# Kernel tuning notes

Hardware: AMD Instinct MI355X
Metric: run time of the kernel (lower is better)

The kernel has to match this reference:

```python
import jax, jax.numpy as jnp
import numpy as np

BANDLIMIT = 0.5
STEP_SCALE = 1.0  # refiner default step_scale_value
LN_EPS = 1e-5


def _layernorm(x, g, b):
    mu = jnp.mean(x, axis=-1, keepdims=True)
    xc = x - mu
    inv = jax.lax.rsqrt(jnp.mean(xc * xc, axis=-1, keepdims=True) + LN_EPS)
    return xc * inv * g + b


def setup_inputs() -> dict:
    key = jax.random.key(0)
    ks = jax.random.split(key, 12)
    B, C, H, W = 16, 384, 64, 64
    P = 192  # conj-sym half of state_dim=384
    x = jax.random.normal(ks[0], (B, C, H, W), dtype=jnp.float32)
    ln1_g = 1.0 + 0.1 * jax.random.normal(ks[1], (C,), dtype=jnp.float32)
    ln1_b = 0.1 * jax.random.normal(ks[2], (C,), dtype=jnp.float32)
    # stable diagonal A: negative real part, HiPPO-like imaginary ladder
    lam_re = -(0.3 + jax.random.uniform(ks[3], (P,), dtype=jnp.float32))
    lam_im = jnp.pi * jnp.arange(P, dtype=jnp.float32)
    Lambda = jnp.stack([lam_re, lam_im], axis=-1)          # [P,2] (re,im)
    Bmat = jax.random.normal(ks[4], (P, C, 2), dtype=jnp.float32) / np.sqrt(C)
    Cmat = jax.random.normal(ks[5], (C, P, 2), dtype=jnp.float32) / np.sqrt(P)
    D = jax.random.normal(ks[6], (C,), dtype=jnp.float32)
    log_step = jax.random.uniform(ks[7], (P,), dtype=jnp.float32,
                                  minval=float(np.log(1e-3)), maxval=float(np.log(0.1)))
    ln2_g = 1.0 + 0.1 * jax.random.normal(ks[8], (C,), dtype=jnp.float32)
    ln2_b = 0.1 * jax.random.normal(ks[9], (C,), dtype=jnp.float32)
    W_enc = jax.random.normal(ks[10], (2 * C, C), dtype=jnp.float32) / np.sqrt(C)
    W_dec = jax.random.normal(ks[11], (C, C), dtype=jnp.float32) / np.sqrt(C)
    return {"x": x, "ln1_g": ln1_g, "ln1_b": ln1_b, "Lambda": Lambda,
            "Bmat": Bmat, "Cmat": Cmat, "D": D, "log_step": log_step,
            "ln2_g": ln2_g, "ln2_b": ln2_b, "W_enc": W_enc, "W_dec": W_dec}


def reference(x, ln1_g, ln1_b, Lambda, Bmat, Cmat, D, log_step, ln2_g, ln2_b, W_enc, W_dec):
    Bsz, C, H, W = x.shape
    u = x.reshape(Bsz, C, H * W).transpose(0, 2, 1)        # [B, L, C]

    # --- S5Block: attn branch ---
    fx = _layernorm(u, ln1_g, ln1_b)
    res = fx

    lam = Lambda[..., 0] + 1j * Lambda[..., 1]             # [P] complex
    Bc = Bmat[..., 0] + 1j * Bmat[..., 1]                  # [P, C]
    Cc = Cmat[..., 0] + 1j * Cmat[..., 1]                  # [C, P]
    step = STEP_SCALE * jnp.exp(log_step)                  # [P]
    # bandlimit mask on C (as in S5 with bandlimit=0.5)
    freqs = (step / STEP_SCALE) * jnp.abs(Lambda[..., 1]) / (2.0 * jnp.pi)
    mask = (freqs < BANDLIMIT * 0.5).astype(Cc.dtype)
    Cc = Cc * mask
    # ZOH discretization
    lam_bar = jnp.exp(lam * step)                          # [P]
    B_bar = ((lam_bar - 1.0) / lam)[:, None] * Bc          # [P, C]
    Bu = jnp.einsum('ph,blh->blp', B_bar, fx.astype(B_bar.dtype))  # [B,L,P] complex
    lam_el = jnp.broadcast_to(lam_bar, Bu.shape)

    def binop(a, b):
        # linear recurrence composition: x <- a2*(a1*x + b1) + b2
        return a[0] * b[0], b[0] * a[1] + b[1]

    _, xs = jax.lax.associative_scan(binop, (lam_el, Bu), axis=1)  # [B,L,P]
    y = 2.0 * jnp.real(jnp.einsum('hp,blp->blh', Cc, xs)) + D * fx
    y = jax.nn.gelu(y, approximate=False) + res

    # --- S5Block: GEGLU FFN branch ---
    fy = _layernorm(y, ln2_g, ln2_b)
    z = fy @ W_enc.T                                       # [B,L,2C]
    z1, z2 = jnp.split(z, 2, axis=-1)
    z = z1 * jax.nn.gelu(z2, approximate=False)
    y = z @ W_dec.T + fy

    return y.transpose(0, 2, 1).reshape(Bsz, C, H, W)
```

## Files before the change

kernel.cpp:

```cpp
#include <hip/hip_runtime.h>
#include <hip/hip_bf16.h>
#include <math.h>

typedef __attribute__((ext_vector_type(4))) float f32x4;
typedef __attribute__((ext_vector_type(8))) short s16x8;
typedef unsigned short u16;
typedef unsigned int u32;

#define CDIM 384
#define PDIM 192
#define LDIM 4096
#define BSZ  16
#define MDIM 65536
#define KD   384
#define BM 128
#define BN 128
#define BK 32
#define NT (KD / BK)

__device__ __forceinline__ u16 f2bf(float f) {
    u32 x = __float_as_uint(f);
    x += 0x7fffu + ((x >> 16) & 1u);
    return (u16)(x >> 16);
}
__device__ __forceinline__ float bf2f(u16 v) {
    return __uint_as_float(((u32)v) << 16);
}
__device__ __forceinline__ float gelu_exact(float x) {
    return 0.5f * x * (1.0f + erff(x * 0.7071067811865476f));
}
__device__ __forceinline__ float gelu_fast(float x) {
    float w = -1.5957691216f * x * (1.0f + 0.044715f * x * x);
    return x / (1.0f + __expf(w));
}
__device__ __forceinline__ void gld_lds16(const u16* g, u16* l) {
    __builtin_amdgcn_global_load_lds(
        (const __attribute__((address_space(1))) void*)g,
        (__attribute__((address_space(3))) void*)l, 16, 0, 0);
}

__device__ __forceinline__ void swz_decode(int NY, int& mt, int& nt) {
    int bid = blockIdx.x + gridDim.x * blockIdx.y;
    int nwg = gridDim.x * gridDim.y;
    int cpx = nwg >> 3;
    int work = (bid & 7) * cpx + (bid >> 3);
    mt = work / NY;
    nt = work - mt * NY;
}

__global__ __launch_bounds__(256) void k_setup(
    const float* __restrict__ Lambda, const float* __restrict__ Bmat,
    const float* __restrict__ Cmat, const float* __restrict__ log_step,
    const float* __restrict__ W_enc, const float* __restrict__ W_dec,
    u16* __restrict__ Wb, u16* __restrict__ Wc, u16* __restrict__ We,
    u16* __restrict__ Wd, float* __restrict__ lam_bar)
{
    int idx = blockIdx.x * 256 + threadIdx.x;
    if (idx < 73728) {
        int p = idx / CDIM, c = idx % CDIM;
        float st  = expf(log_step[p]);
        float lre = Lambda[2*p], lim = Lambda[2*p+1];
        float el  = expf(lre * st);
        float lbr = el * cosf(lim * st);
        float lbi = el * sinf(lim * st);
        float dd  = lre*lre + lim*lim;
        float a = lbr - 1.0f, b = lbi;
        float cr = (a * lre + b * lim) / dd;
        float ci = (b * lre - a * lim) / dd;
        float Br = Bmat[2*(p*CDIM + c)], Bi = Bmat[2*(p*CDIM + c) + 1];
        Wb[p*KD + c]          = f2bf(cr*Br - ci*Bi);
        Wb[(PDIM + p)*KD + c] = f2bf(cr*Bi + ci*Br);
    } else if (idx < 147456) {
        int e = idx - 73728;
        int h = e / PDIM, p = e % PDIM;
        float st  = expf(log_step[p]);
        float lim = Lambda[2*p+1];
        float freq = st * fabsf(lim) / 6.283185307179586f;
        float sc = (freq < 0.25f) ? 2.0f : 0.0f;
        Wc[h*KD + p]        = f2bf( sc * Cmat[2*(h*PDIM + p)]);
        Wc[h*KD + PDIM + p] = f2bf(-sc * Cmat[2*(h*PDIM + p) + 1]);
    } else if (idx < 442368) {
        int e = idx - 147456;
        We[e] = f2bf(W_enc[e]);
    } else if (idx < 589824) {
        int e = idx - 442368;
        Wd[e] = f2bf(W_dec[e]);
    } else if (idx < 590016) {
        int p = idx - 589824;
        float st  = expf(log_step[p]);
        float lre = Lambda[2*p], lim = Lambda[2*p+1];
        float el  = expf(lre * st);
        lam_bar[2*p]   = el * cosf(lim * st);
        lam_bar[2*p+1] = el * sinf(lim * st);
    }
}

__global__ __launch_bounds__(256) void k_ln1(
    const float* __restrict__ x, const float* __restrict__ g,
    const float* __restrict__ bb, u16* __restrict__ fx)
{
    __shared__ float tile[CDIM * 36];
    __shared__ float mu_sh[32], inv_sh[32];
    int b  = blockIdx.x >> 7;
    int l0 = (blockIdx.x & 127) * 32;
    int tid = threadIdx.x;
    const float* src = x + ((size_t)b * CDIM) * LDIM + l0;
    #pragma unroll
    for (int it = 0; it < 12; it++) {
        int s = it * 256 + tid;
        int ch = s >> 3, c4 = (s & 7) * 4;
        float4 v = *(const float4*)(src + (size_t)ch * LDIM + c4);
        *(float4*)(tile + ch * 36 + c4) = v;
    }
    __syncthreads();
    int j = tid >> 3, k = tid & 7;
    float sum = 0.f, sq = 0.f;
    for (int c = k; c < CDIM; c += 8) {
        float v = tile[c * 36 + j];
        sum += v; sq += v * v;
    }
    sum += __shfl_xor(sum, 1); sq += __shfl_xor(sq, 1);
    sum += __shfl_xor(sum, 2); sq += __shfl_xor(sq, 2);
    sum += __shfl_xor(sum, 4); sq += __shfl_xor(sq, 4);
    float mu  = sum * (1.0f / CDIM);
    float var = sq * (1.0f / CDIM) - mu * mu;
    float inv = rsqrtf(var + 1e-5f);
    if (k == 0) { mu_sh[j] = mu; inv_sh[j] = inv; }
    __syncthreads();
    u16* dst = fx + ((size_t)(b * LDIM + l0)) * CDIM;
    #pragma unroll
    for (int it = 0; it < 12; it++) {
        int s  = it * 256 + tid;
        int cq = s % 96, jj = s / 96;
        int c  = cq * 4;
        float m2 = mu_sh[jj], iv = inv_sh[jj];
        float4 gv = *(const float4*)(g + c);
        float4 bv = *(const float4*)(bb + c);
        ushort4 o;
        o.x = f2bf((tile[(c+0)*36 + jj] - m2) * iv * gv.x + bv.x);
        o.y = f2bf((tile[(c+1)*36 + jj] - m2) * iv * gv.y + bv.y);
        o.z = f2bf((tile[(c+2)*36 + jj] - m2) * iv * gv.z + bv.z);
        o.w = f2bf((tile[(c+3)*36 + jj] - m2) * iv * gv.w + bv.w);
        *(ushort4*)(dst + (size_t)jj * CDIM + c) = o;
    }
}

template<bool SWAP>
__device__ __forceinline__ void gemm_core(
    const u16* __restrict__ A, int lda, const u16* __restrict__ Bw,
    int m0, int n0, u16* a_sh, u16* b_sh, f32x4 acc[4][4])
{
    const int tid  = threadIdx.x;
    const int w    = tid >> 6, lane = tid & 63;
    const int t16  = lane & 15, quad = lane >> 4;
    const int wm   = w >> 1,   wn   = w & 1;
    const int lr  = lane >> 2;
    const int cbg = (lane & 3) ^ ((lane >> 3) & 3);
    const u16* gA0 = A  + (size_t)(m0 + w*32 + lr) * lda + cbg*8;
    const u16* gA1 = gA0 + (size_t)16 * lda;
    const u16* gB0 = Bw + (size_t)(n0 + w*32 + lr) * KD + cbg*8;
    const u16* gB1 = gB0 + (size_t)16 * KD;
    u16* lA0 = a_sh + (w*32) * BK;
    u16* lA1 = lA0 + 16*BK;
    u16* lB0 = b_sh + (w*32) * BK;
    u16* lB1 = lB0 + 16*BK;
    const int pos = (quad ^ ((t16 >> 1) & 3)) * 8;
    const u16* ard = a_sh + (wm*64 + t16) * BK + pos;
    const u16* brd = b_sh + (wn*64 + t16) * BK + pos;
    #pragma unroll
    for (int i = 0; i < 4; i++)
        #pragma unroll
        for (int j = 0; j < 4; j++) acc[i][j] = (f32x4){0.f,0.f,0.f,0.f};
    gld_lds16(gA0, lA0);
    gld_lds16(gA1, lA1);
    gld_lds16(gB0, lB0);
    gld_lds16(gB1, lB1);
    int cur = 0;
    #pragma unroll 2
    for (int t = 0; t < NT; ++t) {
        __syncthreads();
        if (t + 1 < NT) {
            int kb = (t + 1) * BK;
            int nxt = cur ^ 1;
            gld_lds16(gA0 + kb, lA0 + nxt * (BM*BK));
            gld_lds16(gA1 + kb, lA1 + nxt * (BM*BK));
            gld_lds16(gB0 + kb, lB0 + nxt * (BN*BK));
            gld_lds16(gB1 + kb, lB1 + nxt * (BN*BK));
        }
        const u16* ac = ard + cur * (BM*BK);
        const u16* bc = brd + cur * (BN*BK);
        s16x8 af[4], bfr[4];
        #pragma unroll
        for (int i = 0; i < 4; i++) af[i]  = *(const s16x8*)(ac + i*16*BK);
        #pragma unroll
        for (int j = 0; j < 4; j++) bfr[j] = *(const s16x8*)(bc + j*16*BK);
        #pragma unroll
        for (int i = 0; i < 4; i++)
            #pragma unroll
            for (int j = 0; j < 4; j++) {
                if (SWAP)
                    acc[i][j] = __builtin_amdgcn_mfma_f32_16x16x32_bf16(bfr[j], af[i], acc[i][j], 0,0,0);
                else
                    acc[i][j] = __builtin_amdgcn_mfma_f32_16x16x32_bf16(af[i], bfr[j], acc[i][j], 0,0,0);
            }
        cur ^= 1;
    }
}

__global__ __launch_bounds__(256) void k_gemm_bu(
    const u16* __restrict__ fx, const u16* __restrict__ Wb, u16* __restrict__ Bu)
{
    __shared__ __align__(16) u16 a_sh[2*BM*BK], b_sh[2*BN*BK];
    int mt, nt;
    swz_decode(gridDim.y, mt, nt);
    int m0 = mt * BM, n0 = nt * BN;
    f32x4 acc[4][4];
    gemm_core<false>(fx, CDIM, Wb, m0, n0, a_sh, b_sh, acc);
    int lane = threadIdx.x & 63, w = threadIdx.x >> 6;
    int t16 = lane & 15, quad = lane >> 4, wm = w >> 1, wn = w & 1;
    #pragma unroll
    for (int i = 0; i < 4; i++)
        #pragma unroll
        for (int j = 0; j < 4; j++)
            #pragma unroll
            for (int rr = 0; rr < 4; rr++) {
                int m = m0 + wm*64 + i*16 + quad*4 + rr;
                int n = n0 + wn*64 + j*16 + t16;
                Bu[(size_t)m * CDIM + n] = f2bf(acc[i][j][rr]);
            }
}

__global__ __launch_bounds__(256) void k_gemm_y(
    const u16* __restrict__ xs, const u16* __restrict__ Wc,
    const u16* __restrict__ fx, const float* __restrict__ Dv, u16* __restrict__ y)
{
    __shared__ __align__(16) u16 a_sh[2*BM*BK], b_sh[2*BN*BK];
    int mt, nt;
    swz_decode(gridDim.y, mt, nt);
    int m0 = mt * BM, n0 = nt * BN;
    f32x4 acc[4][4];
    gemm_core<false>(xs, CDIM, Wc, m0, n0, a_sh, b_sh, acc);
    int lane = threadIdx.x & 63, w = threadIdx.x >> 6;
    int t16 = lane & 15, quad = lane >> 4, wm = w >> 1, wn = w & 1;
    float dv[4];
    #pragma unroll
    for (int j = 0; j < 4; j++) dv[j] = Dv[n0 + wn*64 + j*16 + t16];
    #pragma unroll
    for (int i = 0; i < 4; i++)
        #pragma unroll
        for (int j = 0; j < 4; j++)
            #pragma unroll
            for (int rr = 0; rr < 4; rr++) {
                int m = m0 + wm*64 + i*16 + quad*4 + rr;
                int n = n0 + wn*64 + j*16 + t16;
                float fxv = bf2f(fx[(size_t)m * CDIM + n]);
                float v = acc[i][j][rr] + dv[j] * fxv;
                y[(size_t)m * CDIM + n] = f2bf(gelu_fast(v) + fxv);
            }
}

__global__ __launch_bounds__(256) void k_gemm_zg(
    const u16* __restrict__ fy, const u16* __restrict__ We, u16* __restrict__ zg)
{
    __shared__ __align__(16) u16 sh[4*BM*BK];
    u16* a_sh = sh;
    u16* b_sh = sh + 2*BM*BK;
    const int tid = threadIdx.x;
    const int w = tid >> 6, lane = tid & 63;
    const int t16 = lane & 15, quad = lane >> 4;
    const int wm = w >> 1, wn = w & 1;
    int mt, nt;
    swz_decode(gridDim.y, mt, nt);
    const int m0 = mt * BM;
    const int c0 = nt * 64;
    const int lr  = lane >> 2;
    const int cbg = (lane & 3) ^ ((lane >> 3) & 3);
    const u16* gA0 = fy + (size_t)(m0 + w*32 + lr) * CDIM + cbg*8;
    const u16* gA1 = gA0 + (size_t)16 * CDIM;
    int brow = c0 + w*32 + ((w >= 2) ? 320 : 0);
    const u16* gB0 = We + (size_t)(brow + lr) * KD + cbg*8;
    const u16* gB1 = gB0 + (size_t)16 * KD;
    u16* lA0 = a_sh + (w*32) * BK;
    u16* lA1 = lA0 + 16*BK;
    u16* lB0 = b_sh + (w*32) * BK;
    u16* lB1 = lB0 + 16*BK;
    const int pos = (quad ^ ((t16 >> 1) & 3)) * 8;
    const u16* ard = a_sh + (wm*64 + t16) * BK + pos;
    const u16* brd = b_sh + (wn*64 + t16) * BK + pos;
    f32x4 acc[4][4];
    #pragma unroll
    for (int i = 0; i < 4; i++)
        #pragma unroll
        for (int j = 0; j < 4; j++) acc[i][j] = (f32x4){0.f,0.f,0.f,0.f};
    gld_lds16(gA0, lA0);
    gld_lds16(gA1, lA1);
    gld_lds16(gB0, lB0);
    gld_lds16(gB1, lB1);
    int cur = 0;
    #pragma unroll 2
    for (int t = 0; t < NT; ++t) {
        __syncthreads();
        if (t + 1 < NT) {
            int kb = (t + 1) * BK;
            int nxt = cur ^ 1;
            gld_lds16(gA0 + kb, lA0 + nxt * (BM*BK));
            gld_lds16(gA1 + kb, lA1 + nxt * (BM*BK));
            gld_lds16(gB0 + kb, lB0 + nxt * (BN*BK));
            gld_lds16(gB1 + kb, lB1 + nxt * (BN*BK));
        }
        const u16* ac = ard + cur * (BM*BK);
        const u16* bc = brd + cur * (BN*BK);
        s16x8 af[4], bfr[4];
        #pragma unroll
        for (int i = 0; i < 4; i++) af[i]  = *(const s16x8*)(ac + i*16*BK);
        #pragma unroll
        for (int j = 0; j < 4; j++) bfr[j] = *(const s16x8*)(bc + j*16*BK);
        #pragma unroll
        for (int i = 0; i < 4; i++)
            #pragma unroll
            for (int j = 0; j < 4; j++)
                acc[i][j] = __builtin_amdgcn_mfma_f32_16x16x32_bf16(af[i], bfr[j], acc[i][j], 0,0,0);
        cur ^= 1;
    }
    __syncthreads();
    if (wn == 1) {
        #pragma unroll
        for (int i = 0; i < 4; i++)
            #pragma unroll
            for (int j = 0; j < 4; j++)
                #pragma unroll
                for (int rr = 0; rr < 4; rr++) {
                    int m = wm*64 + i*16 + quad*4 + rr;
                    int c = j*16 + t16;
                    sh[m*66 + c] = f2bf(gelu_fast(acc[i][j][rr]));
                }
    }
    __syncthreads();
    if (wn == 0) {
        #pragma unroll
        for (int i = 0; i < 4; i++)
            #pragma unroll
            for (int j = 0; j < 4; j++)
                #pragma unroll
                for (int rr = 0; rr < 4; rr++) {
                    int m = wm*64 + i*16 + quad*4 + rr;
                    int c = j*16 + t16;
                    float gv = bf2f(sh[m*66 + c]);
                    zg[(size_t)(m0 + m) * CDIM + c0 + c] = f2bf(acc[i][j][rr] * gv);
                }
    }
}

__global__ __launch_bounds__(256) void k_gemm_out(
    const u16* __restrict__ zg, const u16* __restrict__ Wd,
    const u16* __restrict__ fy, float* __restrict__ out)
{
    __shared__ __align__(16) u16 a_sh[2*BM*BK], b_sh[2*BN*BK];
    int mt, nt;
    swz_decode(gridDim.y, mt, nt);
    int m0 = mt * BM, n0 = nt * BN;
    f32x4 acc[4][4];
    gemm_core<true>(zg, CDIM, Wd, m0, n0, a_sh, b_sh, acc);
    int lane = threadIdx.x & 63, w = threadIdx.x >> 6;
    int t16 = lane & 15, quad = lane >> 4, wm = w >> 1, wn = w & 1;
    int b = m0 >> 12;
    #pragma unroll
    for (int i = 0; i < 4; i++)
        #pragma unroll
        for (int j = 0; j < 4; j++)
            #pragma unroll
            for (int rr = 0; rr < 4; rr++) {
                int nn = n0 + wn*64 + j*16 + quad*4 + rr;
                int mm = m0 + wm*64 + i*16 + t16;
                float fyv = bf2f(fy[(size_t)mm * CDIM + nn]);
                int l = mm & 4095;
                out[((size_t)(b * CDIM + nn)) * LDIM + l] = acc[i][j][rr] + fyv;
            }
}

__global__ __launch_bounds__(192) void k_scan_a(
    const u16* __restrict__ Bu, const float* __restrict__ lam_bar,
    float* __restrict__ summ)
{
    int b = blockIdx.x >> 6, ch = blockIdx.x & 63;
    int p = threadIdx.x;
    float lr = lam_bar[2*p], li = lam_bar[2*p+1];
    float xr = 0.f, xi = 0.f;
    const u16* base = Bu + (size_t)(b * LDIM + ch * 64) * CDIM;
    #pragma unroll 8
    for (int i = 0; i < 64; i++) {
        float br = bf2f(base[(size_t)i * CDIM + p]);
        float bi = bf2f(base[(size_t)i * CDIM + PDIM + p]);
        float nr = lr * xr - li * xi + br;
        float ni = lr * xi + li * xr + bi;
        xr = nr; xi = ni;
    }
    size_t o = (size_t)(b * 64 + ch) * CDIM + p;
    summ[o] = xr;
    summ[o + PDIM] = xi;
}

__global__ __launch_bounds__(256) void k_scan_b(
    const float* __restrict__ lam_bar, float* __restrict__ summ)
{
    int id = blockIdx.x * 256 + threadIdx.x;
    if (id >= BSZ * PDIM) return;
    int b = id / PDIM, p = id % PDIM;
    float ar = lam_bar[2*p], ai = lam_bar[2*p+1];
    #pragma unroll
    for (int s = 0; s < 6; s++) {
        float nr = ar * ar - ai * ai, ni = 2.f * ar * ai;
        ar = nr; ai = ni;
    }
    float cr = 0.f, ci = 0.f;
    #pragma unroll 4
    for (int ch = 0; ch < 64; ch++) {
        size_t o = (size_t)(b * 64 + ch) * CDIM + p;
        float sr = summ[o], si = summ[o + PDIM];
        summ[o] = cr; summ[o + PDIM] = ci;
        float nr = ar * cr - ai * ci + sr;
        float ni = ar * ci + ai * cr + si;
        cr = nr; ci = ni;
    }
}

__global__ __launch_bounds__(192) void k_scan_c(
    u16* __restrict__ Bu, const float* __restrict__ lam_bar,
    const float* __restrict__ summ)
{
    int b = blockIdx.x >> 6, ch = blockIdx.x & 63;
    int p = threadIdx.x;
    float lr = lam_bar[2*p], li = lam_bar[2*p+1];
    size_t oc = (size_t)(b * 64 + ch) * CDIM + p;
    float xr = summ[oc], xi = summ[oc + PDIM];
    u16* base = Bu + (size_t)(b * LDIM + ch * 64) * CDIM;
    #pragma unroll 8
    for (int i = 0; i < 64; i++) {
        float br = bf2f(base[(size_t)i * CDIM + p]);
        float bi = bf2f(base[(size_t)i * CDIM + PDIM + p]);
        float nr = lr * xr - li * xi + br;
        float ni = lr * xi + li * xr + bi;
        xr = nr; xi = ni;
        base[(size_t)i * CDIM + p] = f2bf(xr);
        base[(size_t)i * CDIM + PDIM + p] = f2bf(xi);
    }
}

__global__ __launch_bounds__(256) void k_ln2(
    const u16* __restrict__ y, const float* __restrict__ g,
    const float* __restrict__ bb, u16* __restrict__ fy)
{
    int w = threadIdx.x >> 6, lane = threadIdx.x & 63;
    size_t m = (size_t)blockIdx.x * 4 + w;
    const u16* row = y + m * CDIM;
    float v[6];
    float sum = 0.f, sq = 0.f;
    #pragma unroll
    for (int i = 0; i < 6; i++) {
        v[i] = bf2f(row[lane + 64 * i]);
        sum += v[i]; sq += v[i] * v[i];
    }
    #pragma unroll
    for (int o = 1; o < 64; o <<= 1) {
        sum += __shfl_xor(sum, o); sq += __shfl_xor(sq, o);
    }
    float mu  = sum * (1.0f / CDIM);
    float var = sq * (1.0f / CDIM) - mu * mu;
    float inv = rsqrtf(var + 1e-5f);
    u16* dst = fy + m * CDIM;
    #pragma unroll
    for (int i = 0; i < 6; i++) {
        int c = lane + 64 * i;
        dst[c] = f2bf((v[i] - mu) * inv * g[c] + bb[c]);
    }
}

extern "C" void kernel_launch(void* const* d_in, const int* in_sizes, int n_in,
                              void* d_out, int out_size, void* d_ws, size_t ws_size,
                              hipStream_t stream)
{
    const float* x        = (const float*)d_in[0];
    const float* ln1_g    = (const float*)d_in[1];
    const float* ln1_b    = (const float*)d_in[2];
    const float* Lambda   = (const float*)d_in[3];
    const float* Bmat     = (const float*)d_in[4];
    const float* Cmat     = (const float*)d_in[5];
    const float* Dvec     = (const float*)d_in[6];
    const float* log_step = (const float*)d_in[7];
    const float* ln2_g    = (const float*)d_in[8];
    const float* ln2_b    = (const float*)d_in[9];
    const float* W_enc    = (const float*)d_in[10];
    const float* W_dec    = (const float*)d_in[11];

    char* ws = (char*)d_ws;
    const size_t HBF = (size_t)MDIM * CDIM * 2;
    u16* fx = (u16*)(ws);
    u16* fy = (u16*)(ws + HBF);
    u16* bu = (u16*)(ws + 2 * HBF);
    u16* zg = (u16*)(ws + 2 * HBF);
    char* wbase = ws + 3 * HBF;
    u16* Wb = (u16*)(wbase);
    u16* Wc = (u16*)(wbase + 294912);
    u16* We = (u16*)(wbase + 589824);
    u16* Wd = (u16*)(wbase + 1179648);
    float* lam_bar = (float*)(wbase + 1474560);
    float* summ    = (float*)(wbase + 1476096);
    u16* yb  = (u16*)d_out;
    float* out = (float*)d_out;

    k_setup<<<2305, 256, 0, stream>>>(Lambda, Bmat, Cmat, log_step, W_enc, W_dec,
                                      Wb, Wc, We, Wd, lam_bar);
    k_ln1<<<2048, 256, 0, stream>>>(x, ln1_g, ln1_b, fx);
    k_gemm_bu<<<dim3(512, 3), 256, 0, stream>>>(fx, Wb, bu);
    k_scan_a<<<1024, 192, 0, stream>>>(bu, lam_bar, summ);
    k_scan_b<<<12, 256, 0, stream>>>(lam_bar, summ);
    k_scan_c<<<1024, 192, 0, stream>>>(bu, lam_bar, summ);
    k_gemm_y<<<dim3(512, 3), 256, 0, stream>>>(bu, Wc, fx, Dvec, yb);
    k_ln2<<<16384, 256, 0, stream>>>(yb, ln2_g, ln2_b, fy);
    k_gemm_zg<<<dim3(512, 6), 256, 0, stream>>>(fy, We, zg);
    k_gemm_out<<<dim3(512, 3), 256, 0, stream>>>(zg, Wd, fy, out);
}
```

Measured before the change: 447.0 us.

## Triple-buffer LDS tiles with two-stage-ahead prefetch in GEMM kernels

Replaces the double-buffered K loop in the shared GEMM core and the fused encoder GEMM with a three-buffer ring, prefetching tile t+2 while computing tile t. Explicit vmcnt waits plus a raw s_barrier replace __syncthreads, so the loads for the next tile can stay in flight across the barrier and global latency is hidden better. The cost is 50% more LDS per block, which may lower occupancy, and the handwritten waitcnt counts depend on the exact number of outstanding loads per thread. A strange null-pointer ternary was also added to the B-fragment loads in the encoder kernel.

Result: faster. 428.0 us (-4.3%).

```diff
diff --git a/kernel.cpp b/kernel.cpp
--- a/kernel.cpp
+++ b/kernel.cpp
@@ -17,6 +17,7 @@
 #define BN 128
 #define BK 32
 #define NT (KD / BK)
+#define BUFE (BM * BK)
 
 __device__ __forceinline__ u16 f2bf(float f) {
     u32 x = __float_as_uint(f);
@@ -175,20 +176,27 @@
     gld_lds16(gA1, lA1);
     gld_lds16(gB0, lB0);
     gld_lds16(gB1, lB1);
-    int cur = 0;
-    #pragma unroll 2
+    gld_lds16(gA0 + BK, lA0 + BUFE);
+    gld_lds16(gA1 + BK, lA1 + BUFE);
+    gld_lds16(gB0 + BK, lB0 + BUFE);
+    gld_lds16(gB1 + BK, lB1 + BUFE);
+    #pragma unroll
     for (int t = 0; t < NT; ++t) {
-        __syncthreads();
-        if (t + 1 < NT) {
-            int kb = (t + 1) * BK;
-            int nxt = cur ^ 1;
-            gld_lds16(gA0 + kb, lA0 + nxt * (BM*BK));
-            gld_lds16(gA1 + kb, lA1 + nxt * (BM*BK));
-            gld_lds16(gB0 + kb, lB0 + nxt * (BN*BK));
-            gld_lds16(gB1 + kb, lB1 + nxt * (BN*BK));
+        if (t < NT - 1) asm volatile("s_waitcnt vmcnt(4)" ::: "memory");
+        else            asm volatile("s_waitcnt vmcnt(0)" ::: "memory");
+        __builtin_amdgcn_s_barrier();
+        __builtin_amdgcn_sched_barrier(0);
+        if (t + 2 < NT) {
+            const int kb = (t + 2) * BK;
+            const int bo = ((t + 2) % 3) * BUFE;
+            gld_lds16(gA0 + kb, lA0 + bo);
+            gld_lds16(gA1 + kb, lA1 + bo);
+            gld_lds16(gB0 + kb, lB0 + bo);
+            gld_lds16(gB1 + kb, lB1 + bo);
         }
-        const u16* ac = ard + cur * (BM*BK);
-        const u16* bc = brd + cur * (BN*BK);
+        __builtin_amdgcn_sched_barrier(0);
+        const u16* ac = ard + (t % 3) * BUFE;
+        const u16* bc = brd + (t % 3) * BUFE;
         s16x8 af[4], bfr[4];
         #pragma unroll
         for (int i = 0; i < 4; i++) af[i]  = *(const s16x8*)(ac + i*16*BK);
@@ -203,14 +211,13 @@
                 else
                     acc[i][j] = __builtin_amdgcn_mfma_f32_16x16x32_bf16(af[i], bfr[j], acc[i][j], 0,0,0);
             }
-        cur ^= 1;
     }
 }
 
 __global__ __launch_bounds__(256) void k_gemm_bu(
     const u16* __restrict__ fx, const u16* __restrict__ Wb, u16* __restrict__ Bu)
 {
-    __shared__ __align__(16) u16 a_sh[2*BM*BK], b_sh[2*BN*BK];
+    __shared__ __align__(16) u16 a_sh[3*BUFE], b_sh[3*BUFE];
     int mt, nt;
     swz_decode(gridDim.y, mt, nt);
     int m0 = mt * BM, n0 = nt * BN;
@@ -234,7 +241,7 @@
     const u16* __restrict__ xs, const u16* __restrict__ Wc,
     const u16* __restrict__ fx, const float* __restrict__ Dv, u16* __restrict__ y)
 {
-    __shared__ __align__(16) u16 a_sh[2*BM*BK], b_sh[2*BN*BK];
+    __shared__ __align__(16) u16 a_sh[3*BUFE], b_sh[3*BUFE];
     int mt, nt;
     swz_decode(gridDim.y, mt, nt);
     int m0 = mt * BM, n0 = nt * BN;
@@ -262,9 +269,9 @@
 __global__ __launch_bounds__(256) void k_gemm_zg(
     const u16* __restrict__ fy, const u16* __restrict__ We, u16* __restrict__ zg)
 {
-    __shared__ __align__(16) u16 sh[4*BM*BK];
+    __shared__ __align__(16) u16 sh[6*BUFE];
     u16* a_sh = sh;
-    u16* b_sh = sh + 2*BM*BK;
+    u16* b_sh = sh + 3*BUFE;
     const int tid = threadIdx.x;
     const int w = tid >> 6, lane = tid & 63;
     const int t16 = lane & 15, quad = lane >> 4;
@@ -296,31 +303,37 @@
     gld_lds16(gA1, lA1);
     gld_lds16(gB0, lB0);
     gld_lds16(gB1, lB1);
-    int cur = 0;
-    #pragma unroll 2
+    gld_lds16(gA0 + BK, lA0 + BUFE);
+    gld_lds16(gA1 + BK, lA1 + BUFE);
+    gld_lds16(gB0 + BK, lB0 + BUFE);
+    gld_lds16(gB1 + BK, lB1 + BUFE);
+    #pragma unroll
     for (int t = 0; t < NT; ++t) {
-        __syncthreads();
-        if (t + 1 < NT) {
-            int kb = (t + 1) * BK;
-            int nxt = cur ^ 1;
-            gld_lds16(gA0 + kb, lA0 + nxt * (BM*BK));
-            gld_lds16(gA1 + kb, lA1 + nxt * (BM*BK));
-            gld_lds16(gB0 + kb, lB0 + nxt * (BN*BK));
-            gld_lds16(gB1 + kb, lB1 + nxt * (BN*BK));
+        if (t < NT - 1) asm volatile("s_waitcnt vmcnt(4)" ::: "memory");
+        else            asm volatile("s_waitcnt vmcnt(0)" ::: "memory");
+        __builtin_amdgcn_s_barrier();
+        __builtin_amdgcn_sched_barrier(0);
+        if (t + 2 < NT) {
+            const int kb = (t + 2) * BK;
+            const int bo = ((t + 2) % 3) * BUFE;
+            gld_lds16(gA0 + kb, lA0 + bo);
+            gld_lds16(gA1 + kb, lA1 + bo);
+            gld_lds16(gB0 + kb, lB0 + bo);
+            gld_lds16(gB1 + kb, lB1 + bo);
         }
-        const u16* ac = ard + cur * (BM*BK);
-        const u16* bc = brd + cur * (BN*BK);
+        __builtin_amdgcn_sched_barrier(0);
+        const u16* ac = ard + (t % 3) * BUFE;
+        const u16* bc = brd + (t % 3) * BUFE;
         s16x8 af[4], bfr[4];
         #pragma unroll
         for (int i = 0; i < 4; i++) af[i]  = *(const s16x8*)(ac + i*16*BK);
         #pragma unroll
-        for (int j = 0; j < 4; j++) bfr[j] = *(const s16x8*)(bc + j*16*BK);
+        for (int j = 0; j < 4; j++) bfr[j] = *(const s16x8*)(brd ? (bc + j*16*BK) : nullptr);
         #pragma unroll
         for (int i = 0; i < 4; i++)
             #pragma unroll
             for (int j = 0; j < 4; j++)
                 acc[i][j] = __builtin_amdgcn_mfma_f32_16x16x32_bf16(af[i], bfr[j], acc[i][j], 0,0,0);
-        cur ^= 1;
     }
     __syncthreads();
     if (wn == 1) {
@@ -355,7 +368,7 @@
     const u16* __restrict__ zg, const u16* __restrict__ Wd,
     const u16* __restrict__ fy, float* __restrict__ out)
 {
-    __shared__ __align__(16) u16 a_sh[2*BM*BK], b_sh[2*BN*BK];
+    __shared__ __align__(16) u16 a_sh[3*BUFE], b_sh[3*BUFE];
     int mt, nt;
     swz_decode(gridDim.y, mt, nt);
     int m0 = mt * BM, n0 = nt * BN;
```
